# Kernel tuning notes

Measured on AMD Instinct MI355X. Metric: run time of the kernel, lower is better.

## Reference

```python
import jax, jax.numpy as jnp
import numpy as np

DIM, D_STATE, D_CONV, EXPAND = 512, 16, 4, 2
D_INNER = EXPAND * DIM            # 1024
DT_RANK = (DIM + 15) // 16        # 32
B, L = 2, 2048


def setup_inputs() -> dict:
    key = jax.random.key(0)
    ks = jax.random.split(key, 12)
    s_in = 1.0 / np.sqrt(DIM)
    s_xp = 1.0 / np.sqrt(D_INNER)
    s_dt = 1.0 / np.sqrt(DT_RANK)
    return {
        "x": jax.random.normal(ks[0], (B, L, DIM), jnp.float32),
        "ln_g": jnp.ones((DIM,), jnp.float32),
        "ln_b": jnp.zeros((DIM,), jnp.float32),
        "W_in": jax.random.normal(ks[1], (2 * D_INNER, DIM), jnp.float32) * s_in,
        "conv_w": jax.random.normal(ks[2], (D_INNER, D_CONV), jnp.float32) * 0.5,
        "conv_b": jax.random.normal(ks[3], (D_INNER,), jnp.float32) * 0.1,
        "W_xproj": jax.random.normal(ks[4], (DT_RANK + 2 * D_STATE, D_INNER), jnp.float32) * s_xp,
        "W_dt": jax.random.normal(ks[5], (D_INNER, DT_RANK), jnp.float32) * s_dt,
        "b_dt": jax.random.normal(ks[6], (D_INNER,), jnp.float32) * 0.1 - 4.0,  # softplus -> small dt
        "A_log": jnp.log(jax.random.uniform(ks[7], (D_INNER, D_STATE), jnp.float32, 1.0, 16.0)),
        "Dp": jax.random.normal(ks[8], (D_INNER,), jnp.float32),
        "W_out": jax.random.normal(ks[9], (DIM, D_INNER), jnp.float32) * s_xp,
    }


def _layernorm(x, g, b, eps=1e-5):
    mu = jnp.mean(x, -1, keepdims=True)
    var = jnp.mean(jnp.square(x - mu), -1, keepdims=True)
    return (x - mu) * jax.lax.rsqrt(var + eps) * g + b


def reference(x, ln_g, ln_b, W_in, conv_w, conv_b, W_xproj, W_dt, b_dt, A_log, Dp, W_out):
    h = _layernorm(x, ln_g, ln_b)
    # input projection -> [B,L,2*d_inner]
    xz = jnp.einsum('bld,ed->ble', h, W_in)
    xp, z = jnp.split(xz, 2, axis=-1)
    # depthwise causal conv1d over time (kernel d_conv), then SiLU
    xp_pad = jnp.pad(xp, ((0, 0), (D_CONV - 1, 0), (0, 0)))
    xc = conv_b
    for k in range(D_CONV):
        xc = xc + xp_pad[:, k:k + L, :] * conv_w[:, k]
    xc = jax.nn.silu(xc)
    # x_proj -> dt, B, C
    proj = jnp.einsum('bld,ed->ble', xc, W_xproj)
    dt_r = proj[..., :DT_RANK]
    Bm = proj[..., DT_RANK:DT_RANK + D_STATE]          # [B,L,n]
    Cm = proj[..., DT_RANK + D_STATE:]                 # [B,L,n]
    dt = jax.nn.softplus(jnp.einsum('blr,dr->bld', dt_r, W_dt) + b_dt)  # [B,L,d]
    A = -jnp.exp(A_log)                                # [d,n]
    dA = jnp.exp(jnp.einsum('bld,dn->bldn', dt, A))    # [B,L,d,n]
    dBx = dt[..., None] * Bm[:, :, None, :] * xc[..., None]  # [B,L,d,n]
    # selective scan over time (time-major for lax.scan)
    def step(s, inp):
        dA_t, dBx_t, C_t = inp
        s = s * dA_t + dBx_t                           # [B,d,n]
        y_t = jnp.einsum('bdn,bn->bd', s, C_t)
        return s, y_t
    s0 = jnp.zeros((B, D_INNER, D_STATE), xc.dtype)
    _, ys = jax.lax.scan(step, s0,
                         (jnp.moveaxis(dA, 1, 0), jnp.moveaxis(dBx, 1, 0), jnp.moveaxis(Cm, 1, 0)))
    y = jnp.moveaxis(ys, 0, 1)                         # [B,L,d]
    y = y + xc * Dp
    y = y * jax.nn.silu(z)
    out = jnp.einsum('bld,ed->ble', y, W_out)
    return x + out  # dropout is identity in eval mode
```

## Files before the change

### kernel.cpp

```cpp
#include <hip/hip_runtime.h>
#include <hip/hip_bf16.h>
#include <math.h>

#define B_      2
#define L_      2048
#define DIM_    512
#define DINNER  1024
#define DTRANK  32
#define DSTATE  16
#define DCONV   4
#define BL      (B_ * L_)
#define NCHUNK  64
#define CLEN    (L_ / NCHUNK)

typedef __attribute__((ext_vector_type(8))) short bf16x8;
typedef __attribute__((ext_vector_type(4))) float f32x4;

static __device__ __forceinline__ unsigned short f2bf(float f) {
  __hip_bfloat16 h = __float2bfloat16(f);
  return *(unsigned short*)&h;
}
static __device__ __forceinline__ float bf2f(unsigned short u) {
  return __uint_as_float(((unsigned int)u) << 16);
}

static __device__ __forceinline__ void gload16(const void* g, void* l) {
  __builtin_amdgcn_global_load_lds(
      (const __attribute__((address_space(1))) void*)g,
      (__attribute__((address_space(3))) void*)l, 16, 0, 0);
}

__global__ __launch_bounds__(256) void cvt_ln_kernel(
    const float* __restrict__ s0, const float* __restrict__ s1,
    const float* __restrict__ s2, __hip_bfloat16* __restrict__ d0,
    __hip_bfloat16* __restrict__ d1, __hip_bfloat16* __restrict__ d2,
    const float* __restrict__ x, const float* __restrict__ g,
    const float* __restrict__ b, __hip_bfloat16* __restrict__ h) {
  int blk = blockIdx.x;
  if (blk < 1600) {
    int i = (blk * 256 + threadIdx.x) * 4;
    const float* s; __hip_bfloat16* d; int off;
    if (i < 1048576)            { s = s0; d = d0; off = i; }
    else if (i < 1048576+65536) { s = s1; d = d1; off = i - 1048576; }
    else                        { s = s2; d = d2; off = i - 1114112; }
    float4 v = *(const float4*)(s + off);
    d[off + 0] = __float2bfloat16(v.x);
    d[off + 1] = __float2bfloat16(v.y);
    d[off + 2] = __float2bfloat16(v.z);
    d[off + 3] = __float2bfloat16(v.w);
    return;
  }
  int row = (blk - 1600) * 4 + (threadIdx.x >> 6);
  int lane = threadIdx.x & 63;
  const float* xr = x + (size_t)row * DIM_;
  float v[8];
  float sum = 0.f;
#pragma unroll
  for (int i = 0; i < 8; i++) { v[i] = xr[lane + i * 64]; sum += v[i]; }
#pragma unroll
  for (int o = 32; o > 0; o >>= 1) sum += __shfl_xor(sum, o, 64);
  float mu = sum * (1.f / DIM_);
  float vs = 0.f;
#pragma unroll
  for (int i = 0; i < 8; i++) { float dd = v[i] - mu; vs += dd * dd; }
#pragma unroll
  for (int o = 32; o > 0; o >>= 1) vs += __shfl_xor(vs, o, 64);
  float rstd = rsqrtf(vs * (1.f / DIM_) + 1e-5f);
  __hip_bfloat16* hr = h + (size_t)row * DIM_;
#pragma unroll
  for (int i = 0; i < 8; i++) {
    int c = lane + i * 64;
    hr[c] = __float2bfloat16((v[i] - mu) * rstd * g[c] + b[c]);
  }
}

template <bool ADD_RES, bool OUT_BF16>
__global__ __launch_bounds__(256) void gemm_mfma_128(
    const __hip_bfloat16* __restrict__ A, int lda,
    const __hip_bfloat16* __restrict__ Bw, int ldb,
    const float* __restrict__ Res, int ldr,
    void* __restrict__ C, int ldc, int K) {
  __shared__ short As[128 * 64];
  __shared__ short Bs[128 * 64];
  int t = threadIdx.x;
  int n0 = blockIdx.x * 128, m0 = blockIdx.y * 128;
  int w = t >> 6, lane = t & 63;
  int wm = (w >> 1) * 64, wn = (w & 1) * 64;
  int l15 = lane & 15, quad = lane >> 4;
  int lr = lane >> 3, lc = (lane & 7) * 8;
  const short* Ag = (const short*)A + (size_t)(m0 + w * 32 + lr) * lda + lc;
  const short* Bg = (const short*)Bw + (size_t)(n0 + w * 32 + lr) * ldb + lc;
  f32x4 acc[4][4];
#pragma unroll
  for (int i = 0; i < 4; i++)
#pragma unroll
    for (int j = 0; j < 4; j++) acc[i][j] = (f32x4){0.f, 0.f, 0.f, 0.f};
  for (int k0 = 0; k0 < K; k0 += 64) {
    __syncthreads();
#pragma unroll
    for (int p = 0; p < 4; p++) {
      gload16(Ag + (size_t)(p * 8) * lda + k0, &As[(w * 32 + p * 8) * 64]);
      gload16(Bg + (size_t)(p * 8) * ldb + k0, &Bs[(w * 32 + p * 8) * 64]);
    }
    __syncthreads();
#pragma unroll
    for (int kk = 0; kk < 64; kk += 32) {
      bf16x8 af[4], bfr[4];
#pragma unroll
      for (int i = 0; i < 4; i++) {
        af[i] = *(const bf16x8*)&As[(wm + i * 16 + l15) * 64 + kk + quad * 8];
        bfr[i] = *(const bf16x8*)&Bs[(wn + i * 16 + l15) * 64 + kk + quad * 8];
      }
#pragma unroll
      for (int i = 0; i < 4; i++)
#pragma unroll
        for (int j = 0; j < 4; j++)
          acc[i][j] = __builtin_amdgcn_mfma_f32_16x16x32_bf16(
              af[i], bfr[j], acc[i][j], 0, 0, 0);
    }
  }
#pragma unroll
  for (int i = 0; i < 4; i++)
#pragma unroll
    for (int r = 0; r < 4; r++) {
      int row = m0 + wm + i * 16 + quad * 4 + r;
#pragma unroll
      for (int j = 0; j < 4; j++) {
        int col = n0 + wn + j * 16 + l15;
        float v = acc[i][j][r];
        if (ADD_RES) v += Res[(size_t)row * ldr + col];
        if (OUT_BF16)
          ((unsigned short*)C)[(size_t)row * ldc + col] = f2bf(v);
        else
          ((float*)C)[(size_t)row * ldc + col] = v;
      }
    }
}

template <bool ADD_RES>
__global__ __launch_bounds__(256) void gemm_mfma_64(
    const __hip_bfloat16* __restrict__ A, int lda,
    const __hip_bfloat16* __restrict__ Bw, int ldb,
    const float* __restrict__ Res, int ldr,
    float* __restrict__ C, int ldc, int K, size_t czs) {
  __shared__ short As[64 * 64];
  __shared__ short Bs[64 * 64];
  int t = threadIdx.x;
  int n0 = blockIdx.x * 64, m0 = blockIdx.y * 64;
  size_t kbase = (size_t)blockIdx.z * K;
  int w = t >> 6, lane = t & 63;
  int wm = (w >> 1) * 32, wn = (w & 1) * 32;
  int l15 = lane & 15, quad = lane >> 4;
  int lr = lane >> 3, lc = (lane & 7) * 8;
  const short* Ag = (const short*)A + (size_t)(m0 + w * 16 + lr) * lda + lc + kbase;
  const short* Bg = (const short*)Bw + (size_t)(n0 + w * 16 + lr) * ldb + lc + kbase;
  f32x4 acc[2][2];
#pragma unroll
  for (int i = 0; i < 2; i++)
#pragma unroll
    for (int j = 0; j < 2; j++) acc[i][j] = (f32x4){0.f, 0.f, 0.f, 0.f};
  for (int k0 = 0; k0 < K; k0 += 64) {
    __syncthreads();
#pragma unroll
    for (int p = 0; p < 2; p++) {
      gload16(Ag + (size_t)(p * 8) * lda + k0, &As[(w * 16 + p * 8) * 64]);
      gload16(Bg + (size_t)(p * 8) * ldb + k0, &Bs[(w * 16 + p * 8) * 64]);
    }
    __syncthreads();
#pragma unroll
    for (int kk = 0; kk < 64; kk += 32) {
      bf16x8 af[2], bfr[2];
#pragma unroll
      for (int i = 0; i < 2; i++) {
        af[i] = *(const bf16x8*)&As[(wm + i * 16 + l15) * 64 + kk + quad * 8];
        bfr[i] = *(const bf16x8*)&Bs[(wn + i * 16 + l15) * 64 + kk + quad * 8];
      }
#pragma unroll
      for (int i = 0; i < 2; i++)
#pragma unroll
        for (int j = 0; j < 2; j++)
          acc[i][j] = __builtin_amdgcn_mfma_f32_16x16x32_bf16(
              af[i], bfr[j], acc[i][j], 0, 0, 0);
    }
  }
  float* Cz = C + czs * blockIdx.z;
#pragma unroll
  for (int i = 0; i < 2; i++)
#pragma unroll
    for (int r = 0; r < 4; r++) {
      int row = m0 + wm + i * 16 + quad * 4 + r;
#pragma unroll
      for (int j = 0; j < 2; j++) {
        int col = n0 + wn + j * 16 + l15;
        float v = acc[i][j][r];
        if (ADD_RES) v += Res[(size_t)row * ldr + col];
        Cz[(size_t)row * ldc + col] = v;
      }
    }
}

__global__ __launch_bounds__(256) void conv_silu_kernel(
    const unsigned short* __restrict__ xzb, const float* __restrict__ cw,
    const float* __restrict__ cb, __hip_bfloat16* __restrict__ xc_bf) {
  int idx = blockIdx.x * 256 + threadIdx.x;
  int d4 = (idx & 255) * 4;
  int bl = idx >> 8;
  int l = bl & (L_ - 1);
  const unsigned short* base = xzb + (size_t)bl * 2048 + d4;
  float4 acc = *(const float4*)(cb + d4);
  float4 w0 = *(const float4*)(cw + (d4 + 0) * 4);
  float4 w1 = *(const float4*)(cw + (d4 + 1) * 4);
  float4 w2 = *(const float4*)(cw + (d4 + 2) * 4);
  float4 w3 = *(const float4*)(cw + (d4 + 3) * 4);
  if (l >= 3) {
    ushort4 r = *(const ushort4*)(base - 3 * 2048);
    acc.x += bf2f(r.x) * w0.x; acc.y += bf2f(r.y) * w1.x;
    acc.z += bf2f(r.z) * w2.x; acc.w += bf2f(r.w) * w3.x;
  }
  if (l >= 2) {
    ushort4 r = *(const ushort4*)(base - 2 * 2048);
    acc.x += bf2f(r.x) * w0.y; acc.y += bf2f(r.y) * w1.y;
    acc.z += bf2f(r.z) * w2.y; acc.w += bf2f(r.w) * w3.y;
  }
  if (l >= 1) {
    ushort4 r = *(const ushort4*)(base - 1 * 2048);
    acc.x += bf2f(r.x) * w0.z; acc.y += bf2f(r.y) * w1.z;
    acc.z += bf2f(r.z) * w2.z; acc.w += bf2f(r.w) * w3.z;
  }
  {
    ushort4 r = *(const ushort4*)(base);
    acc.x += bf2f(r.x) * w0.w; acc.y += bf2f(r.y) * w1.w;
    acc.z += bf2f(r.z) * w2.w; acc.w += bf2f(r.w) * w3.w;
  }
  float4 v;
  v.x = acc.x / (1.f + __expf(-acc.x));
  v.y = acc.y / (1.f + __expf(-acc.y));
  v.z = acc.z / (1.f + __expf(-acc.z));
  v.w = acc.w / (1.f + __expf(-acc.w));
  ushort4 hb;
  hb.x = f2bf(v.x); hb.y = f2bf(v.y); hb.z = f2bf(v.z); hb.w = f2bf(v.w);
  *(ushort4*)(xc_bf + (size_t)bl * DINNER + d4) = hb;
}

__global__ __launch_bounds__(256) void dt_kernel(
    const float* __restrict__ pp, float* __restrict__ proj,
    const float* __restrict__ Wdt, const float* __restrict__ bdt,
    float* __restrict__ dt) {
  int blk = blockIdx.x;
  int dgrp = blk & 3;
  int bl0 = (blk >> 2) * 16;
  int d = dgrp * 256 + threadIdx.x;
  __shared__ float pr[16 * 64];
  for (int i = threadIdx.x; i < 16 * 64; i += 256) {
    size_t o = (size_t)bl0 * 64 + i;
    float v = pp[o] + pp[o + 262144] + pp[o + 2 * 262144] + pp[o + 3 * 262144];
    pr[i] = v;
    if (dgrp == 0) proj[o] = v;
  }
  float w[32];
#pragma unroll
  for (int r4 = 0; r4 < 8; r4++) {
    float4 wv = *(const float4*)(Wdt + (size_t)d * 32 + r4 * 4);
    w[r4 * 4 + 0] = wv.x; w[r4 * 4 + 1] = wv.y;
    w[r4 * 4 + 2] = wv.z; w[r4 * 4 + 3] = wv.w;
  }
  float bias = bdt[d];
  __syncthreads();
#pragma unroll
  for (int row = 0; row < 16; row++) {
    float a0 = 0.f, a1 = 0.f, a2 = 0.f, a3 = 0.f;
#pragma unroll
    for (int r4 = 0; r4 < 8; r4++) {
      float4 pv = *(const float4*)&pr[row * 64 + r4 * 4];
      a0 = fmaf(pv.x, w[r4 * 4 + 0], a0);
      a1 = fmaf(pv.y, w[r4 * 4 + 1], a1);
      a2 = fmaf(pv.z, w[r4 * 4 + 2], a2);
      a3 = fmaf(pv.w, w[r4 * 4 + 3], a3);
    }
    float acc = bias + ((a0 + a1) + (a2 + a3));
    float sp = (acc > 20.f) ? acc : __logf(1.f + __expf(acc));
    dt[(size_t)(bl0 + row) * DINNER + d] = sp;
  }
}

__global__ __launch_bounds__(256) void scan1_kernel(
    const float* __restrict__ dt, const __hip_bfloat16* __restrict__ xc_bf,
    const float* __restrict__ proj, const float* __restrict__ A_log,
    float* __restrict__ T, float* __restrict__ E) {
  int bid = blockIdx.x;
  int dgrp = bid & 63;
  int c = (bid >> 6) & (NCHUNK - 1);
  int b = bid >> 12;
  int tid = threadIdx.x;
  int n = tid & 15;
  int dl = tid >> 4;
  int d = dgrp * 16 + dl;
  int l0 = c * CLEN;
  __shared__ float dts[CLEN * 16];
  __shared__ float dxs[CLEN * 16];
  __shared__ float Bsh[CLEN * 16];
  for (int i = tid; i < CLEN * 16; i += 256) {
    int row = i >> 4, col = i & 15;
    size_t bl = (size_t)(b * L_ + l0 + row);
    float dtv = dt[bl * DINNER + dgrp * 16 + col];
    float xv = __bfloat162float(xc_bf[bl * DINNER + dgrp * 16 + col]);
    dts[i] = dtv;
    dxs[i] = dtv * xv;
    Bsh[i] = proj[bl * 64 + 32 + col];
  }
  float Aa = -__expf(A_log[(size_t)d * 16 + n]);
  __syncthreads();
  float Tn = 1.f, En = 0.f;
#pragma unroll 8
  for (int l = 0; l < CLEN; l++) {
    float dA = __expf(dts[l * 16 + dl] * Aa);
    Tn *= dA;
    En = En * dA + dxs[l * 16 + dl] * Bsh[l * 16 + n];
  }
  size_t o = (((size_t)b * NCHUNK + c) * DINNER + d) * 16 + n;
  T[o] = Tn; E[o] = En;
}

__global__ __launch_bounds__(256) void combine_kernel(
    float* __restrict__ T, const float* __restrict__ E) {
  int idx = blockIdx.x * 256 + threadIdx.x;
  int b = idx >> 14;
  int dn = idx & 16383;
  size_t base = (size_t)b * NCHUNK * (DINNER * 16) + dn;
  float s = 0.f;
#pragma unroll
  for (int batch = 0; batch < 4; batch++) {
    float t[16], e[16];
#pragma unroll
    for (int j = 0; j < 16; j++) {
      size_t o = base + (size_t)(batch * 16 + j) * (DINNER * 16);
      t[j] = T[o]; e[j] = E[o];
    }
#pragma unroll
    for (int j = 0; j < 16; j++) {
      T[base + (size_t)(batch * 16 + j) * (DINNER * 16)] = s;
      s = t[j] * s + e[j];
    }
  }
}

__global__ __launch_bounds__(256) void scan2_kernel(
    const float* __restrict__ dt, const __hip_bfloat16* __restrict__ xc_bf,
    const float* __restrict__ proj, const float* __restrict__ A_log,
    const float* __restrict__ Sstart, const float* __restrict__ Dp,
    unsigned short* __restrict__ xzb) {
  int bid = blockIdx.x;
  int dgrp = bid & 3;
  int c = (bid >> 2) & (NCHUNK - 1);
  int b = bid >> 8;
  int d = dgrp * 256 + threadIdx.x;
  int l0 = c * CLEN;
  __shared__ float Bs[CLEN * 16];
  __shared__ float Cs[CLEN * 16];
  for (int i = threadIdx.x; i < CLEN * 16; i += 256) {
    int row = i >> 4, nn = i & 15;
    const float* pr = proj + (size_t)(b * L_ + l0 + row) * 64;
    Bs[i] = pr[32 + nn];
    Cs[i] = pr[48 + nn];
  }
  float Aa[16], s[16];
  size_t sb = (((size_t)b * NCHUNK + c) * DINNER + d) * 16;
#pragma unroll
  for (int q = 0; q < 4; q++) {
    float4 av = *(const float4*)(A_log + (size_t)d * 16 + q * 4);
    Aa[q * 4 + 0] = -__expf(av.x); Aa[q * 4 + 1] = -__expf(av.y);
    Aa[q * 4 + 2] = -__expf(av.z); Aa[q * 4 + 3] = -__expf(av.w);
    float4 sv = *(const float4*)(Sstart + sb + q * 4);
    s[q * 4 + 0] = sv.x; s[q * 4 + 1] = sv.y;
    s[q * 4 + 2] = sv.z; s[q * 4 + 3] = sv.w;
  }
  float Dv = Dp[d];
  __syncthreads();
  for (int l = l0; l < l0 + CLEN; l++) {
    int bl = b * L_ + l;
    float dtv = dt[(size_t)bl * DINNER + d];
    float xv = __bfloat162float(xc_bf[(size_t)bl * DINNER + d]);
    float dx = dtv * xv;
    int lrow = (l - l0) * 16;
    float y = 0.f;
#pragma unroll
    for (int n = 0; n < 16; n++) {
      float dA = __expf(dtv * Aa[n]);
      s[n] = s[n] * dA + dx * Bs[lrow + n];
      y += s[n] * Cs[lrow + n];
    }
    float zv = bf2f(xzb[(size_t)bl * 2048 + 1024 + d]);
    float gate = zv / (1.f + __expf(-zv));
    xzb[(size_t)bl * 2048 + d] = f2bf((y + xv * Dv) * gate);
  }
}

extern "C" void kernel_launch(void* const* d_in, const int* in_sizes, int n_in,
                              void* d_out, int out_size, void* d_ws, size_t ws_size,
                              hipStream_t stream) {
  const float* x      = (const float*)d_in[0];
  const float* ln_g   = (const float*)d_in[1];
  const float* ln_b   = (const float*)d_in[2];
  const float* W_in   = (const float*)d_in[3];
  const float* conv_w = (const float*)d_in[4];
  const float* conv_b = (const float*)d_in[5];
  const float* W_xprj = (const float*)d_in[6];
  const float* W_dt   = (const float*)d_in[7];
  const float* b_dt   = (const float*)d_in[8];
  const float* A_log  = (const float*)d_in[9];
  const float* Dp     = (const float*)d_in[10];
  const float* W_out  = (const float*)d_in[11];
  float* out = (float*)d_out;

  float* ws     = (float*)d_ws;
  float* xzb_f  = ws;
  float* xcbf_f = xzb_f + 4194304;
  float* proj   = xcbf_f + 2097152;
  float* pp     = proj + 262144;
  float* dtb    = pp + 1048576;
  float* T      = dtb + 4194304;
  float* E      = T + 2097152;
  float* hbf_f  = E + 2097152;
  float* wbf    = hbf_f + 1048576;

  unsigned short* xzb   = (unsigned short*)xzb_f;
  __hip_bfloat16* xc_bf = (__hip_bfloat16*)xcbf_f;
  __hip_bfloat16* h_bf  = (__hip_bfloat16*)hbf_f;
  __hip_bfloat16* Wb_in = (__hip_bfloat16*)wbf;
  __hip_bfloat16* Wb_xp = Wb_in + 1048576;
  __hip_bfloat16* Wb_out = Wb_xp + 65536;
  __hip_bfloat16* y_bf  = (__hip_bfloat16*)xzb;

  cvt_ln_kernel<<<1600 + BL / 4, 256, 0, stream>>>(
      W_in, W_xprj, W_out, Wb_in, Wb_xp, Wb_out, x, ln_g, ln_b, h_bf);
  gemm_mfma_128<false, true><<<dim3(2 * DINNER / 128, BL / 128), 256, 0, stream>>>(
      h_bf, DIM_, Wb_in, DIM_, nullptr, 0, xzb, 2 * DINNER, DIM_);
  conv_silu_kernel<<<(BL * DINNER / 4) / 256, 256, 0, stream>>>(
      xzb, conv_w, conv_b, xc_bf);
  gemm_mfma_64<false><<<dim3(1, BL / 64, 4), 256, 0, stream>>>(
      xc_bf, DINNER, Wb_xp, DINNER, nullptr, 0, pp, 64, 256, 262144);
  dt_kernel<<<(BL / 16) * 4, 256, 0, stream>>>(pp, proj, W_dt, b_dt, dtb);
  scan1_kernel<<<B_ * NCHUNK * 64, 256, 0, stream>>>(dtb, xc_bf, proj, A_log, T, E);
  combine_kernel<<<(B_ * DINNER * 16) / 256, 256, 0, stream>>>(T, E);
  scan2_kernel<<<B_ * NCHUNK * 4, 256, 0, stream>>>(dtb, xc_bf, proj, A_log, T, Dp, xzb);
  gemm_mfma_64<true><<<dim3(DIM_ / 64, BL / 64, 1), 256, 0, stream>>>(
      y_bf, 2048, Wb_out, DINNER, x, DIM_, out, DIM_, DINNER, 0);
}
```

Measured before the change: 212.2 us.

## Fuse dt projection into scan kernels and widen x_proj split-K

```diff
diff --git a/kernel.cpp b/kernel.cpp
--- a/kernel.cpp
+++ b/kernel.cpp
@@ -28,6 +28,10 @@
   __builtin_amdgcn_global_load_lds(
       (const __attribute__((address_space(1))) void*)g,
       (__attribute__((address_space(3))) void*)l, 16, 0, 0);
+}
+
+static __device__ __forceinline__ float softplus_f(float acc) {
+  return (acc > 20.f) ? acc : __logf(1.f + __expf(acc));
 }
 
 __global__ __launch_bounds__(256) void cvt_ln_kernel(
@@ -242,51 +246,23 @@
   *(ushort4*)(xc_bf + (size_t)bl * DINNER + d4) = hb;
 }
 
-__global__ __launch_bounds__(256) void dt_kernel(
-    const float* __restrict__ pp, float* __restrict__ proj,
-    const float* __restrict__ Wdt, const float* __restrict__ bdt,
-    float* __restrict__ dt) {
-  int blk = blockIdx.x;
-  int dgrp = blk & 3;
-  int bl0 = (blk >> 2) * 16;
-  int d = dgrp * 256 + threadIdx.x;
-  __shared__ float pr[16 * 64];
-  for (int i = threadIdx.x; i < 16 * 64; i += 256) {
-    size_t o = (size_t)bl0 * 64 + i;
-    float v = pp[o] + pp[o + 262144] + pp[o + 2 * 262144] + pp[o + 3 * 262144];
-    pr[i] = v;
-    if (dgrp == 0) proj[o] = v;
-  }
-  float w[32];
-#pragma unroll
-  for (int r4 = 0; r4 < 8; r4++) {
-    float4 wv = *(const float4*)(Wdt + (size_t)d * 32 + r4 * 4);
-    w[r4 * 4 + 0] = wv.x; w[r4 * 4 + 1] = wv.y;
-    w[r4 * 4 + 2] = wv.z; w[r4 * 4 + 3] = wv.w;
-  }
-  float bias = bdt[d];
-  __syncthreads();
-#pragma unroll
-  for (int row = 0; row < 16; row++) {
-    float a0 = 0.f, a1 = 0.f, a2 = 0.f, a3 = 0.f;
-#pragma unroll
-    for (int r4 = 0; r4 < 8; r4++) {
-      float4 pv = *(const float4*)&pr[row * 64 + r4 * 4];
-      a0 = fmaf(pv.x, w[r4 * 4 + 0], a0);
-      a1 = fmaf(pv.y, w[r4 * 4 + 1], a1);
-      a2 = fmaf(pv.z, w[r4 * 4 + 2], a2);
-      a3 = fmaf(pv.w, w[r4 * 4 + 3], a3);
-    }
-    float acc = bias + ((a0 + a1) + (a2 + a3));
-    float sp = (acc > 20.f) ? acc : __logf(1.f + __expf(acc));
-    dt[(size_t)(bl0 + row) * DINNER + d] = sp;
-  }
+__global__ __launch_bounds__(256) void reduce8_kernel(
+    const float* __restrict__ pp, float* __restrict__ proj) {
+  int i = (blockIdx.x * 256 + threadIdx.x) * 4;
+  float4 s = *(const float4*)(pp + i);
+#pragma unroll
+  for (int k = 1; k < 8; k++) {
+    float4 a = *(const float4*)(pp + i + k * 262144);
+    s.x += a.x; s.y += a.y; s.z += a.z; s.w += a.w;
+  }
+  *(float4*)(proj + i) = s;
 }
 
 __global__ __launch_bounds__(256) void scan1_kernel(
-    const float* __restrict__ dt, const __hip_bfloat16* __restrict__ xc_bf,
-    const float* __restrict__ proj, const float* __restrict__ A_log,
-    float* __restrict__ T, float* __restrict__ E) {
+    const __hip_bfloat16* __restrict__ xc_bf, const float* __restrict__ proj,
+    const float* __restrict__ A_log, const float* __restrict__ Wdt,
+    const float* __restrict__ bdt, float* __restrict__ T,
+    float* __restrict__ E) {
   int bid = blockIdx.x;
   int dgrp = bid & 63;
   int c = (bid >> 6) & (NCHUNK - 1);
@@ -302,11 +278,22 @@
   for (int i = tid; i < CLEN * 16; i += 256) {
     int row = i >> 4, col = i & 15;
     size_t bl = (size_t)(b * L_ + l0 + row);
-    float dtv = dt[bl * DINNER + dgrp * 16 + col];
-    float xv = __bfloat162float(xc_bf[bl * DINNER + dgrp * 16 + col]);
+    int dcol = dgrp * 16 + col;
+    const float* prow = proj + bl * 64;
+    const float* wrow = Wdt + (size_t)dcol * 32;
+    float a0 = 0.f, a1 = 0.f, a2 = 0.f, a3 = 0.f;
+#pragma unroll
+    for (int q = 0; q < 8; q++) {
+      float4 pv = *(const float4*)(prow + q * 4);
+      float4 wv = *(const float4*)(wrow + q * 4);
+      a0 = fmaf(pv.x, wv.x, a0); a1 = fmaf(pv.y, wv.y, a1);
+      a2 = fmaf(pv.z, wv.z, a2); a3 = fmaf(pv.w, wv.w, a3);
+    }
+    float dtv = softplus_f(bdt[dcol] + ((a0 + a1) + (a2 + a3)));
+    float xv = __bfloat162float(xc_bf[bl * DINNER + dcol]);
     dts[i] = dtv;
     dxs[i] = dtv * xv;
-    Bsh[i] = proj[bl * 64 + 32 + col];
+    Bsh[i] = prow[32 + col];
   }
   float Aa = -__expf(A_log[(size_t)d * 16 + n]);
   __syncthreads();
@@ -327,42 +314,57 @@
   int b = idx >> 14;
   int dn = idx & 16383;
   size_t base = (size_t)b * NCHUNK * (DINNER * 16) + dn;
+  float t[64], e[64];
+#pragma unroll
+  for (int j = 0; j < 64; j++) {
+    size_t o = base + (size_t)j * (DINNER * 16);
+    t[j] = T[o]; e[j] = E[o];
+  }
   float s = 0.f;
 #pragma unroll
-  for (int batch = 0; batch < 4; batch++) {
-    float t[16], e[16];
-#pragma unroll
-    for (int j = 0; j < 16; j++) {
-      size_t o = base + (size_t)(batch * 16 + j) * (DINNER * 16);
-      t[j] = T[o]; e[j] = E[o];
-    }
-#pragma unroll
-    for (int j = 0; j < 16; j++) {
-      T[base + (size_t)(batch * 16 + j) * (DINNER * 16)] = s;
-      s = t[j] * s + e[j];
-    }
-  }
+  for (int j = 0; j < 64; j++) {
+    float tj = t[j];
+    t[j] = s;
+    s = tj * s + e[j];
+  }
+#pragma unroll
+  for (int j = 0; j < 64; j++)
+    T[base + (size_t)j * (DINNER * 16)] = t[j];
 }
 
 __global__ __launch_bounds__(256) void scan2_kernel(
-    const float* __restrict__ dt, const __hip_bfloat16* __restrict__ xc_bf,
-    const float* __restrict__ proj, const float* __restrict__ A_log,
-    const float* __restrict__ Sstart, const float* __restrict__ Dp,
-    unsigned short* __restrict__ xzb) {
+    const __hip_bfloat16* __restrict__ xc_bf, const float* __restrict__ proj,
+    const float* __restrict__ A_log, const float* __restrict__ Sstart,
+    const float* __restrict__ Dp, const float* __restrict__ Wdt,
+    const float* __restrict__ bdt, unsigned short* __restrict__ xzb) {
   int bid = blockIdx.x;
   int dgrp = bid & 3;
   int c = (bid >> 2) & (NCHUNK - 1);
   int b = bid >> 8;
-  int d = dgrp * 256 + threadIdx.x;
+  int tid = threadIdx.x;
+  int d = dgrp * 256 + tid;
   int l0 = c * CLEN;
   __shared__ float Bs[CLEN * 16];
   __shared__ float Cs[CLEN * 16];
-  for (int i = threadIdx.x; i < CLEN * 16; i += 256) {
+  __shared__ float Pr[CLEN * 32];
+  for (int i = tid; i < CLEN * 16; i += 256) {
     int row = i >> 4, nn = i & 15;
     const float* pr = proj + (size_t)(b * L_ + l0 + row) * 64;
     Bs[i] = pr[32 + nn];
     Cs[i] = pr[48 + nn];
   }
+  for (int i = tid; i < CLEN * 32; i += 256) {
+    int row = i >> 5, rr = i & 31;
+    Pr[i] = proj[(size_t)(b * L_ + l0 + row) * 64 + rr];
+  }
+  float w[32];
+#pragma unroll
+  for (int q = 0; q < 8; q++) {
+    float4 wv = *(const float4*)(Wdt + (size_t)d * 32 + q * 4);
+    w[q * 4 + 0] = wv.x; w[q * 4 + 1] = wv.y;
+    w[q * 4 + 2] = wv.z; w[q * 4 + 3] = wv.w;
+  }
+  float bias = bdt[d];
   float Aa[16], s[16];
   size_t sb = (((size_t)b * NCHUNK + c) * DINNER + d) * 16;
 #pragma unroll
@@ -376,18 +378,32 @@
   }
   float Dv = Dp[d];
   __syncthreads();
-  for (int l = l0; l < l0 + CLEN; l++) {
-    int bl = b * L_ + l;
-    float dtv = dt[(size_t)bl * DINNER + d];
-    float xv = __bfloat162float(xc_bf[(size_t)bl * DINNER + d]);
+  float dt32[CLEN], xv32[CLEN];
+#pragma unroll
+  for (int l = 0; l < CLEN; l++) {
+    float a0 = 0.f, a1 = 0.f, a2 = 0.f, a3 = 0.f;
+#pragma unroll
+    for (int q = 0; q < 8; q++) {
+      a0 = fmaf(Pr[l * 32 + q * 4 + 0], w[q * 4 + 0], a0);
+      a1 = fmaf(Pr[l * 32 + q * 4 + 1], w[q * 4 + 1], a1);
+      a2 = fmaf(Pr[l * 32 + q * 4 + 2], w[q * 4 + 2], a2);
+      a3 = fmaf(Pr[l * 32 + q * 4 + 3], w[q * 4 + 3], a3);
+    }
+    dt32[l] = softplus_f(bias + ((a0 + a1) + (a2 + a3)));
+    xv32[l] = __bfloat162float(xc_bf[(size_t)(b * L_ + l0 + l) * DINNER + d]);
+  }
+#pragma unroll
+  for (int l = 0; l < CLEN; l++) {
+    int bl = b * L_ + l0 + l;
+    float dtv = dt32[l];
+    float xv = xv32[l];
     float dx = dtv * xv;
-    int lrow = (l - l0) * 16;
     float y = 0.f;
 #pragma unroll
     for (int n = 0; n < 16; n++) {
       float dA = __expf(dtv * Aa[n]);
-      s[n] = s[n] * dA + dx * Bs[lrow + n];
-      y += s[n] * Cs[lrow + n];
+      s[n] = s[n] * dA + dx * Bs[l * 16 + n];
+      y += s[n] * Cs[l * 16 + n];
     }
     float zv = bf2f(xzb[(size_t)bl * 2048 + 1024 + d]);
     float gate = zv / (1.f + __expf(-zv));
@@ -417,8 +433,7 @@
   float* xcbf_f = xzb_f + 4194304;
   float* proj   = xcbf_f + 2097152;
   float* pp     = proj + 262144;
-  float* dtb    = pp + 1048576;
-  float* T      = dtb + 4194304;
+  float* T      = pp + 2097152;
   float* E      = T + 2097152;
   float* hbf_f  = E + 2097152;
   float* wbf    = hbf_f + 1048576;
@@ -437,12 +452,14 @@
       h_bf, DIM_, Wb_in, DIM_, nullptr, 0, xzb, 2 * DINNER, DIM_);
   conv_silu_kernel<<<(BL * DINNER / 4) / 256, 256, 0, stream>>>(
       xzb, conv_w, conv_b, xc_bf);
-  gemm_mfma_64<false><<<dim3(1, BL / 64, 4), 256, 0, stream>>>(
-      xc_bf, DINNER, Wb_xp, DINNER, nullptr, 0, pp, 64, 256, 262144);
-  dt_kernel<<<(BL / 16) * 4, 256, 0, stream>>>(pp, proj, W_dt, b_dt, dtb);
-  scan1_kernel<<<B_ * NCHUNK * 64, 256, 0, stream>>>(dtb, xc_bf, proj, A_log, T, E);
+  gemm_mfma_64<false><<<dim3(1, BL / 64, 8), 256, 0, stream>>>(
+      xc_bf, DINNER, Wb_xp, DINNER, nullptr, 0, pp, 64, 128, 262144);
+  reduce8_kernel<<<256, 256, 0, stream>>>(pp, proj);
+  scan1_kernel<<<B_ * NCHUNK * 64, 256, 0, stream>>>(
+      xc_bf, proj, A_log, W_dt, b_dt, T, E);
   combine_kernel<<<(B_ * DINNER * 16) / 256, 256, 0, stream>>>(T, E);
-  scan2_kernel<<<B_ * NCHUNK * 4, 256, 0, stream>>>(dtb, xc_bf, proj, A_log, T, Dp, xzb);
+  scan2_kernel<<<B_ * NCHUNK * 4, 256, 0, stream>>>(
+      xc_bf, proj, A_log, T, Dp, W_dt, b_dt, xzb);
   gemm_mfma_64<true><<<dim3(DIM_ / 64, BL / 64, 1), 256, 0, stream>>>(
       y_bf, 2048, Wb_out, DINNER, x, DIM_, out, DIM_, DINNER, 0);
 }
```

Result: slower. 236.8 us (+11.6%).
